# Performance work log

Measured on AMD Instinct MI355X. Metric: run time of the kernel, lower is better.

Reference implementation:

```python
import jax, jax.numpy as jnp
import numpy as np

# Production-scale dims (see shape_source)
B, D_MODEL, L = 2, 1024, 8192
NUM_GROUPS = 256          # d_model of ExplicitSingleDecayFilter
L_CACHE = 128             # explicit filter length (padded to L inside fftconv)
LOG_R_MIN, LOG_R_MAX = 0.0, 2.0  # decay_preset='strong'


def setup_inputs() -> dict:
    key = jax.random.key(0)
    k1, k2, k3, k4, k5 = jax.random.split(key, 5)
    x1 = jax.random.normal(k1, (B, D_MODEL, L), jnp.float32)
    x2 = jax.random.normal(k2, (B, D_MODEL, L), jnp.float32)
    v = jax.random.normal(k3, (B, D_MODEL, L), jnp.float32)
    # h init: randn(d_model, L_cache)/sqrt(L_cache) (small_init scale omitted for numerics)
    h = jax.random.normal(k4, (NUM_GROUPS, L_CACHE), jnp.float32) / np.sqrt(L_CACHE).astype(np.float32)
    conv_bias = jax.random.normal(k5, (D_MODEL,), jnp.float32)
    return {"x1": x1, "x2": x2, "v": v, "h": h, "conv_bias": conv_bias}


def _decay_filter(h):
    # ExplicitSingleDecayFilter: k = h * exp(-logspace(r_min, r_max)[:, None] * linspace(0, 1, L_cache)[None])
    G, Lc = h.shape
    t = jnp.linspace(0.0, 1.0, Lc, dtype=h.dtype)[None]                 # [1, Lc]
    decay_domain = jnp.logspace(LOG_R_MIN, LOG_R_MAX, G, dtype=h.dtype)[:, None]  # [G, 1]
    return h * jnp.exp(-decay_domain * t)                               # [G, Lc]


def reference(x1, x2, v, h, conv_bias):
    Bv, D, Lseq = x1.shape
    G = h.shape[0]
    gd = D // G
    fft_size = 2 * Lseq

    # grouped causal FFT convolution of the gated signal z = x2 * v
    z = (x2 * v).reshape(Bv, G, gd, Lseq)
    x1g = x1.reshape(Bv, G, gd, Lseq)

    k = _decay_filter(h)                                    # [G, L_cache]
    k = jnp.pad(k, ((0, 0), (0, Lseq - k.shape[-1])))       # pad filter to seqlen
    # torch: k_f = rfft(k, n)/n ; y = irfft(u_f*k_f, n, norm='forward')[..., :L]
    # which equals numpy-default irfft(rfft(u, n) * rfft(k, n), n)[..., :L]
    k_f = jnp.fft.rfft(k, n=fft_size)                       # [G, L+1] complex
    z_f = jnp.fft.rfft(z, n=fft_size)                       # [B, G, gd, L+1]
    y = jnp.fft.irfft(z_f * k_f[None, :, None, :], n=fft_size)[..., :Lseq]

    # D shortcut term (conv_bias), no gelu, no dropout in this operator
    Dterm = conv_bias.reshape(G, gd)
    out = y + z * Dterm[None, :, :, None]

    # post-gating by x1, back to [B, D, L] then [B, L, D]
    out = (out * x1g).reshape(Bv, D, Lseq)
    return jnp.transpose(out, (0, 2, 1))
```

## Files before the change

kernel.cpp:

```cpp
#include <hip/hip_runtime.h>

typedef float f4  __attribute__((ext_vector_type(4)));
typedef short s8v __attribute__((ext_vector_type(8)));
typedef short s4v __attribute__((ext_vector_type(4)));

#define BB    2
#define DDIM  1024
#define LSEQ  8192
#define LC    128
#define TD    16
#define TL    512
#define HALO  128
#define ZSTR  648
#define OB2   (TL/8)

__device__ __forceinline__ unsigned bf16pk(float lo, float hi) {
    unsigned a = __float_as_uint(lo), b = __float_as_uint(hi);
    a = (a + 0x7FFFu + ((a >> 16) & 1u)) >> 16;
    b = (b + 0x7FFFu + ((b >> 16) & 1u));
    return (a & 0xFFFFu) | (b & 0xFFFF0000u);
}
__device__ __forceinline__ float bf2f(short s) {
    return __uint_as_float(((unsigned)(unsigned short)s) << 16);
}

union U8 { s8v s; unsigned u[4]; };

__global__ __launch_bounds__(256, 4) void hyena_mfma_kernel(
    const float* __restrict__ x1,
    const float* __restrict__ x2,
    const float* __restrict__ v,
    const float* __restrict__ h,
    const float* __restrict__ cb,
    float* __restrict__ out)
{
    __shared__ union SM {
        short zb[TD][ZSTR];
        f4 ob[TD][OB2];
    } sm;

    const int t = threadIdx.x;

    const int flat = blockIdx.x;
    const int xcd  = flat & 7;
    const int rr_  = flat >> 3;
    const int d0   = (rr_ & 63) * TD;
    const int c_   = xcd + 8*(rr_ >> 6);
    const int l0   = (c_ & 15) * TL;
    const int b    = c_ >> 4;

    const int r = t & 15, sbase = t >> 4;
    const size_t rb = ((size_t)(b*DDIM + d0 + r)) * LSEQ;
    f4 xa0[5], xa1[5], xw0[5], xw1[5];
    #pragma unroll
    for (int it = 0; it < 5; ++it) {
        const int gl = l0 - HALO + (sbase + 16*it)*8;
        if (gl >= 0) {
            xa0[it] = *(const f4*)(x2 + rb + gl);
            xa1[it] = *(const f4*)(x2 + rb + gl + 4);
            xw0[it] = *(const f4*)(v  + rb + gl);
            xw1[it] = *(const f4*)(v  + rb + gl + 4);
        }
    }

    #pragma unroll
    for (int it = 0; it < 5; ++it) {
        const int s = sbase + 16*it;
        const int gl = l0 - HALO + s*8;
        U8 zz; zz.s = (s8v){0,0,0,0,0,0,0,0};
        if (gl >= 0) {
            const f4 z0 = xa0[it]*xw0[it], z1 = xa1[it]*xw1[it];
            zz.u[0] = bf16pk(z0[0], z0[1]);
            zz.u[1] = bf16pk(z0[2], z0[3]);
            zz.u[2] = bf16pk(z1[0], z1[1]);
            zz.u[3] = bf16pk(z1[2], z1[3]);
        }
        *(s8v*)&sm.zb[r][s*8] = zz.s;
    }

    const int wv = t >> 6, lane = t & 63;
    const int j  = lane & 15, kb = lane >> 4;
    const int qj = j & 3,  cc = j >> 2;
    const int row = wv*4 + cc;
    const size_t chb = ((size_t)(b*DDIM + d0 + row)) * LSEQ + l0;
    f4 x1r[8];
    #pragma unroll
    for (int ci = 0; ci < 8; ++ci)
        x1r[ci] = *(const f4*)(x1 + chb + 64*ci + 16*qj + 4*kb);
    const float bd = cb[d0 + row];

    const int g = (d0 >> 2) + wv;
    const float* __restrict__ hg = h + g*LC;
    const float dd = __expf((float)g * (2.0f/255.0f) * 2.302585092994046f);
    const float t0 = dd * (1.0f/127.0f);
    const int   M0base = j - 8*kb + 16;
    const float rE = __expf(t0);
    const float sU = __expf(-32.0f*t0);
    float pE[8];
    pE[0] = 1.0f;
    #pragma unroll
    for (int e = 1; e < 8; ++e) pE[e] = pE[e-1]*rE;
    float baseU = __expf(-t0*(float)M0base);

    s8v afr[5];
    #pragma unroll
    for (int u = 0; u < 5; ++u) {
        const int M0 = M0base + 32*u;
        float kv[8];
        #pragma unroll
        for (int e = 0; e < 8; ++e) {
            const int m = M0 - e;
            const int mc = m < 0 ? 0 : (m > 127 ? 127 : m);
            const float hv = hg[mc];
            const float w  = ((unsigned)m < 128u) ? baseU*pE[e] : 0.0f;
            kv[e] = hv * w;
        }
        U8 aa;
        aa.u[0] = bf16pk(kv[0], kv[1]);
        aa.u[1] = bf16pk(kv[2], kv[3]);
        aa.u[2] = bf16pk(kv[4], kv[5]);
        aa.u[3] = bf16pk(kv[6], kv[7]);
        afr[u] = aa.s;
        baseU *= sU;
    }
    __syncthreads();

    f4 ov[8];
    #pragma unroll
    for (int ci = 0; ci < 8; ++ci) {
        const int L = 64*ci + 16*qj;
        f4 acc = {0.f, 0.f, 0.f, 0.f};
        #pragma unroll
        for (int u = 0; u < 5; ++u) {
            int bi = 112 + L + 8*kb - 32*u;
            bi = bi < 0 ? 0 : bi;
            const s8v bf = *(const s8v*)&sm.zb[row][bi];
            acc = __builtin_amdgcn_mfma_f32_16x16x32_bf16(afr[u], bf, acc, 0, 0, 0);
        }
        const int lo = L + 4*kb;
        const s4v z4 = *(const s4v*)&sm.zb[row][HALO + lo];
        f4 o;
        o[0] = (acc[0] + bf2f(z4[0])*bd) * x1r[ci][0];
        o[1] = (acc[1] + bf2f(z4[1])*bd) * x1r[ci][1];
        o[2] = (acc[2] + bf2f(z4[2])*bd) * x1r[ci][2];
        o[3] = (acc[3] + bf2f(z4[3])*bd) * x1r[ci][3];
        ov[ci] = o;
    }

    const int seg = t & 3;
    #pragma unroll
    for (int hp = 0; hp < 2; ++hp) {
        __syncthreads();
        #pragma unroll
        for (int ci = 0; ci < 4; ++ci) {
            const int cidx = hp*4 + ci;
            const int J = (4*cidx + qj)*4 + kb - hp*64;
            sm.ob[row][J ^ (row & 7)] = ov[cidx];
        }
        __syncthreads();
        #pragma unroll
        for (int it = 0; it < 4; ++it) {
            const int ll = (t >> 2) + it*64;
            const int J = ll >> 2, e = ll & 3;
            f4 o;
            #pragma unroll
            for (int rr2 = 0; rr2 < 4; ++rr2) {
                const int r2 = seg*4 + rr2;
                o[rr2] = ((const float*)&sm.ob[r2][J ^ (r2 & 7)])[e];
            }
            __builtin_nontemporal_store(o,
                (f4*)(out + ((size_t)b*LSEQ + l0 + hp*256 + ll)*DDIM + d0 + seg*4));
        }
    }
}

extern "C" void kernel_launch(void* const* d_in, const int* in_sizes, int n_in,
                              void* d_out, int out_size, void* d_ws, size_t ws_size,
                              hipStream_t stream) {
    const float* x1 = (const float*)d_in[0];
    const float* x2 = (const float*)d_in[1];
    const float* v  = (const float*)d_in[2];
    const float* h  = (const float*)d_in[3];
    const float* cb = (const float*)d_in[4];
    float* outp = (float*)d_out;
    hipLaunchKernelGGL(hyena_mfma_kernel, dim3(2048), dim3(256), 0, stream,
                       x1, x2, v, h, cb, outp);
}
```

Before: 50.94 us.

## Split work into single-wave blocks of one channel group each

Each block now handles one 4-channel group with a single 64-thread wavefront instead of 16 channels across four waves. The grid grows from 2048 to 8192 blocks and shared memory per block drops, so more blocks can be resident and the block barriers only synchronise one wave. In exchange, each output store now writes 16 contiguous bytes per row instead of 64, which makes stores less coalesced, and the XOR swizzle on the staging buffer is removed.

```diff
diff --git a/kernel.cpp b/kernel.cpp
--- a/kernel.cpp
+++ b/kernel.cpp
@@ -8,11 +8,10 @@
 #define DDIM  1024
 #define LSEQ  8192
 #define LC    128
-#define TD    16
+#define TD    4
 #define TL    512
 #define HALO  128
 #define ZSTR  648
-#define OB2   (TL/8)
 
 __device__ __forceinline__ unsigned bf16pk(float lo, float hi) {
     unsigned a = __float_as_uint(lo), b = __float_as_uint(hi);
@@ -26,7 +25,7 @@
 
 union U8 { s8v s; unsigned u[4]; };
 
-__global__ __launch_bounds__(256, 4) void hyena_mfma_kernel(
+__global__ __launch_bounds__(64, 4) void hyena_mfma_kernel(
     const float* __restrict__ x1,
     const float* __restrict__ x2,
     const float* __restrict__ v,
@@ -36,7 +35,7 @@
 {
     __shared__ union SM {
         short zb[TD][ZSTR];
-        f4 ob[TD][OB2];
+        f4 ob[TD][64];
     } sm;
 
     const int t = threadIdx.x;
@@ -44,17 +43,18 @@
     const int flat = blockIdx.x;
     const int xcd  = flat & 7;
     const int rr_  = flat >> 3;
-    const int d0   = (rr_ & 63) * TD;
-    const int c_   = xcd + 8*(rr_ >> 6);
+    const int g    = rr_ & 255;
+    const int c_   = xcd + 8*(rr_ >> 8);
     const int l0   = (c_ & 15) * TL;
     const int b    = c_ >> 4;
+    const int d0   = g * 4;
 
-    const int r = t & 15, sbase = t >> 4;
+    const int r = t >> 4, sidx = t & 15;
     const size_t rb = ((size_t)(b*DDIM + d0 + r)) * LSEQ;
     f4 xa0[5], xa1[5], xw0[5], xw1[5];
     #pragma unroll
     for (int it = 0; it < 5; ++it) {
-        const int gl = l0 - HALO + (sbase + 16*it)*8;
+        const int gl = l0 - HALO + (sidx + 16*it)*8;
         if (gl >= 0) {
             xa0[it] = *(const f4*)(x2 + rb + gl);
             xa1[it] = *(const f4*)(x2 + rb + gl + 4);
@@ -65,7 +65,7 @@
 
     #pragma unroll
     for (int it = 0; it < 5; ++it) {
-        const int s = sbase + 16*it;
+        const int s = sidx + 16*it;
         const int gl = l0 - HALO + s*8;
         U8 zz; zz.s = (s8v){0,0,0,0,0,0,0,0};
         if (gl >= 0) {
@@ -78,10 +78,9 @@
         *(s8v*)&sm.zb[r][s*8] = zz.s;
     }
 
-    const int wv = t >> 6, lane = t & 63;
-    const int j  = lane & 15, kb = lane >> 4;
+    const int j  = t & 15, kb = t >> 4;
     const int qj = j & 3,  cc = j >> 2;
-    const int row = wv*4 + cc;
+    const int row = cc;
     const size_t chb = ((size_t)(b*DDIM + d0 + row)) * LSEQ + l0;
     f4 x1r[8];
     #pragma unroll
@@ -89,7 +88,6 @@
         x1r[ci] = *(const f4*)(x1 + chb + 64*ci + 16*qj + 4*kb);
     const float bd = cb[d0 + row];
 
-    const int g = (d0 >> 2) + wv;
     const float* __restrict__ hg = h + g*LC;
     const float dd = __expf((float)g * (2.0f/255.0f) * 2.302585092994046f);
     const float t0 = dd * (1.0f/127.0f);
@@ -147,7 +145,6 @@
         ov[ci] = o;
     }
 
-    const int seg = t & 3;
     #pragma unroll
     for (int hp = 0; hp < 2; ++hp) {
         __syncthreads();
@@ -155,21 +152,19 @@
         for (int ci = 0; ci < 4; ++ci) {
             const int cidx = hp*4 + ci;
             const int J = (4*cidx + qj)*4 + kb - hp*64;
-            sm.ob[row][J ^ (row & 7)] = ov[cidx];
+            sm.ob[row][J] = ov[cidx];
         }
         __syncthreads();
         #pragma unroll
         for (int it = 0; it < 4; ++it) {
-            const int ll = (t >> 2) + it*64;
+            const int ll = t + it*64;
             const int J = ll >> 2, e = ll & 3;
             f4 o;
             #pragma unroll
-            for (int rr2 = 0; rr2 < 4; ++rr2) {
-                const int r2 = seg*4 + rr2;
-                o[rr2] = ((const float*)&sm.ob[r2][J ^ (r2 & 7)])[e];
-            }
+            for (int c2 = 0; c2 < 4; ++c2)
+                o[c2] = ((const float*)&sm.ob[c2][J])[e];
             __builtin_nontemporal_store(o,
-                (f4*)(out + ((size_t)b*LSEQ + l0 + hp*256 + ll)*DDIM + d0 + seg*4));
+                (f4*)(out + ((size_t)b*LSEQ + l0 + hp*256 + ll)*DDIM + d0));
         }
     }
 }
@@ -183,6 +178,6 @@
     const float* h  = (const float*)d_in[3];
     const float* cb = (const float*)d_in[4];
     float* outp = (float*)d_out;
-    hipLaunchKernelGGL(hyena_mfma_kernel, dim3(2048), dim3(256), 0, stream,
+    hipLaunchKernelGGL(hyena_mfma_kernel, dim3(8192), dim3(64), 0, stream,
                        x1, x2, v, h, cb, outp);
 }
```

After: 169.1 us. +232.0%, slower.

## Double sequence tile per block to amortize halo and filter setup

Applied to the files above, without the earlier changes.

Each block now handles a 1024-long sequence tile instead of 512, processed as two 512 sub-tiles that share one staged z buffer and one set of filter fragments. This halves the grid, cuts the redundant 128-sample halo loads per output element, and amortizes the per-block filter construction. The z staging and output transpose buffers are no longer aliased, which raises shared memory per block, and launch bounds drop to 3 blocks per CU. That may reduce occupancy and latency hiding on a memory-bound kernel.

```diff
diff --git a/kernel.cpp b/kernel.cpp
--- a/kernel.cpp
+++ b/kernel.cpp
@@ -9,10 +9,10 @@
 #define LSEQ  8192
 #define LC    128
 #define TD    16
-#define TL    512
+#define TL    1024
 #define HALO  128
-#define ZSTR  648
-#define OB2   (TL/8)
+#define ZSTR  1160
+#define OB2   64
 
 __device__ __forceinline__ unsigned bf16pk(float lo, float hi) {
     unsigned a = __float_as_uint(lo), b = __float_as_uint(hi);
@@ -26,7 +26,7 @@
 
 union U8 { s8v s; unsigned u[4]; };
 
-__global__ __launch_bounds__(256, 4) void hyena_mfma_kernel(
+__global__ __launch_bounds__(256, 3) void hyena_mfma_kernel(
     const float* __restrict__ x1,
     const float* __restrict__ x2,
     const float* __restrict__ v,
@@ -34,10 +34,8 @@
     const float* __restrict__ cb,
     float* __restrict__ out)
 {
-    __shared__ union SM {
-        short zb[TD][ZSTR];
-        f4 ob[TD][OB2];
-    } sm;
+    __shared__ short zb[TD][ZSTR];
+    __shared__ f4    ob[TD][OB2];
 
     const int t = threadIdx.x;
 
@@ -46,50 +44,71 @@
     const int rr_  = flat >> 3;
     const int d0   = (rr_ & 63) * TD;
     const int c_   = xcd + 8*(rr_ >> 6);
-    const int l0   = (c_ & 15) * TL;
-    const int b    = c_ >> 4;
-
-    const int r = t & 15, sbase = t >> 4;
+    const int l0   = (c_ & 7) * TL;
+    const int b    = c_ >> 3;
+
+    const int r = t & 15, sidx = t >> 4;
     const size_t rb = ((size_t)(b*DDIM + d0 + r)) * LSEQ;
-    f4 xa0[5], xa1[5], xw0[5], xw1[5];
-    #pragma unroll
-    for (int it = 0; it < 5; ++it) {
-        const int gl = l0 - HALO + (sbase + 16*it)*8;
-        if (gl >= 0) {
+
+    {
+        f4 xa0[5], xa1[5], xw0[5], xw1[5];
+        #pragma unroll
+        for (int it = 0; it < 5; ++it) {
+            const int gl = l0 - HALO + (sidx + 16*it)*8;
+            if (gl >= 0) {
+                xa0[it] = *(const f4*)(x2 + rb + gl);
+                xa1[it] = *(const f4*)(x2 + rb + gl + 4);
+                xw0[it] = *(const f4*)(v  + rb + gl);
+                xw1[it] = *(const f4*)(v  + rb + gl + 4);
+            }
+        }
+        #pragma unroll
+        for (int it = 0; it < 5; ++it) {
+            const int s = sidx + 16*it;
+            const int gl = l0 - HALO + s*8;
+            U8 zz; zz.s = (s8v){0,0,0,0,0,0,0,0};
+            if (gl >= 0) {
+                const f4 z0 = xa0[it]*xw0[it], z1 = xa1[it]*xw1[it];
+                zz.u[0] = bf16pk(z0[0], z0[1]);
+                zz.u[1] = bf16pk(z0[2], z0[3]);
+                zz.u[2] = bf16pk(z1[0], z1[1]);
+                zz.u[3] = bf16pk(z1[2], z1[3]);
+            }
+            *(s8v*)&zb[r][s*8] = zz.s;
+        }
+    }
+    {
+        f4 xa0[4], xa1[4], xw0[4], xw1[4];
+        #pragma unroll
+        for (int it = 0; it < 4; ++it) {
+            const int gl = l0 - HALO + (sidx + 16*(it+5))*8;
             xa0[it] = *(const f4*)(x2 + rb + gl);
             xa1[it] = *(const f4*)(x2 + rb + gl + 4);
             xw0[it] = *(const f4*)(v  + rb + gl);
             xw1[it] = *(const f4*)(v  + rb + gl + 4);
         }
-    }
-
-    #pragma unroll
-    for (int it = 0; it < 5; ++it) {
-        const int s = sbase + 16*it;
-        const int gl = l0 - HALO + s*8;
-        U8 zz; zz.s = (s8v){0,0,0,0,0,0,0,0};
-        if (gl >= 0) {
+        #pragma unroll
+        for (int it = 0; it < 4; ++it) {
+            const int s = sidx + 16*(it+5);
             const f4 z0 = xa0[it]*xw0[it], z1 = xa1[it]*xw1[it];
+            U8 zz;
             zz.u[0] = bf16pk(z0[0], z0[1]);
             zz.u[1] = bf16pk(z0[2], z0[3]);
             zz.u[2] = bf16pk(z1[0], z1[1]);
             zz.u[3] = bf16pk(z1[2], z1[3]);
-        }
-        *(s8v*)&sm.zb[r][s*8] = zz.s;
+            *(s8v*)&zb[r][s*8] = zz.s;
+        }
     }
 
     const int wv = t >> 6, lane = t & 63;
     const int j  = lane & 15, kb = lane >> 4;
     const int qj = j & 3,  cc = j >> 2;
     const int row = wv*4 + cc;
+    const int seg = t & 3;
     const size_t chb = ((size_t)(b*DDIM + d0 + row)) * LSEQ + l0;
-    f4 x1r[8];
-    #pragma unroll
-    for (int ci = 0; ci < 8; ++ci)
-        x1r[ci] = *(const f4*)(x1 + chb + 64*ci + 16*qj + 4*kb);
     const float bd = cb[d0 + row];
-
     const int g = (d0 >> 2) + wv;
+
     const float* __restrict__ hg = h + g*LC;
     const float dd = __expf((float)g * (2.0f/255.0f) * 2.302585092994046f);
     const float t0 = dd * (1.0f/127.0f);
@@ -125,51 +144,60 @@
     }
     __syncthreads();
 
-    f4 ov[8];
     #pragma unroll
-    for (int ci = 0; ci < 8; ++ci) {
-        const int L = 64*ci + 16*qj;
-        f4 acc = {0.f, 0.f, 0.f, 0.f};
-        #pragma unroll
-        for (int u = 0; u < 5; ++u) {
-            int bi = 112 + L + 8*kb - 32*u;
-            bi = bi < 0 ? 0 : bi;
-            const s8v bf = *(const s8v*)&sm.zb[row][bi];
-            acc = __builtin_amdgcn_mfma_f32_16x16x32_bf16(afr[u], bf, acc, 0, 0, 0);
-        }
-        const int lo = L + 4*kb;
-        const s4v z4 = *(const s4v*)&sm.zb[row][HALO + lo];
-        f4 o;
-        o[0] = (acc[0] + bf2f(z4[0])*bd) * x1r[ci][0];
-        o[1] = (acc[1] + bf2f(z4[1])*bd) * x1r[ci][1];
-        o[2] = (acc[2] + bf2f(z4[2])*bd) * x1r[ci][2];
-        o[3] = (acc[3] + bf2f(z4[3])*bd) * x1r[ci][3];
-        ov[ci] = o;
-    }
-
-    const int seg = t & 3;
-    #pragma unroll
-    for (int hp = 0; hp < 2; ++hp) {
-        __syncthreads();
-        #pragma unroll
-        for (int ci = 0; ci < 4; ++ci) {
-            const int cidx = hp*4 + ci;
-            const int J = (4*cidx + qj)*4 + kb - hp*64;
-            sm.ob[row][J ^ (row & 7)] = ov[cidx];
-        }
-        __syncthreads();
-        #pragma unroll
-        for (int it = 0; it < 4; ++it) {
-            const int ll = (t >> 2) + it*64;
-            const int J = ll >> 2, e = ll & 3;
+    for (int sub = 0; sub < 2; ++sub) {
+        const int SL = sub * 512;
+
+        f4 x1r[8];
+        #pragma unroll
+        for (int ci = 0; ci < 8; ++ci)
+            x1r[ci] = *(const f4*)(x1 + chb + SL + 64*ci + 16*qj + 4*kb);
+
+        f4 ov[8];
+        #pragma unroll
+        for (int ci = 0; ci < 8; ++ci) {
+            const int L = SL + 64*ci + 16*qj;
+            f4 acc = {0.f, 0.f, 0.f, 0.f};
+            #pragma unroll
+            for (int u = 0; u < 5; ++u) {
+                int bi = 112 + L + 8*kb - 32*u;
+                bi = bi < 0 ? 0 : bi;
+                const s8v bf = *(const s8v*)&zb[row][bi];
+                acc = __builtin_amdgcn_mfma_f32_16x16x32_bf16(afr[u], bf, acc, 0, 0, 0);
+            }
+            const int lo = L + 4*kb;
+            const s4v z4 = *(const s4v*)&zb[row][HALO + lo];
             f4 o;
+            o[0] = (acc[0] + bf2f(z4[0])*bd) * x1r[ci][0];
+            o[1] = (acc[1] + bf2f(z4[1])*bd) * x1r[ci][1];
+            o[2] = (acc[2] + bf2f(z4[2])*bd) * x1r[ci][2];
+            o[3] = (acc[3] + bf2f(z4[3])*bd) * x1r[ci][3];
+            ov[ci] = o;
+        }
+
+        #pragma unroll
+        for (int hp = 0; hp < 2; ++hp) {
+            __syncthreads();
             #pragma unroll
-            for (int rr2 = 0; rr2 < 4; ++rr2) {
-                const int r2 = seg*4 + rr2;
-                o[rr2] = ((const float*)&sm.ob[r2][J ^ (r2 & 7)])[e];
-            }
-            __builtin_nontemporal_store(o,
-                (f4*)(out + ((size_t)b*LSEQ + l0 + hp*256 + ll)*DDIM + d0 + seg*4));
+            for (int ci = 0; ci < 4; ++ci) {
+                const int cidx = hp*4 + ci;
+                const int J = (4*cidx + qj)*4 + kb - hp*64;
+                ob[row][J ^ (row & 7)] = ov[cidx];
+            }
+            __syncthreads();
+            #pragma unroll
+            for (int it = 0; it < 4; ++it) {
+                const int ll = (t >> 2) + it*64;
+                const int J = ll >> 2, e = ll & 3;
+                f4 o;
+                #pragma unroll
+                for (int rr2 = 0; rr2 < 4; ++rr2) {
+                    const int r2 = seg*4 + rr2;
+                    o[rr2] = ((const float*)&ob[r2][J ^ (r2 & 7)])[e];
+                }
+                __builtin_nontemporal_store(o,
+                    (f4*)(out + ((size_t)b*LSEQ + l0 + SL + hp*256 + ll)*DDIM + d0 + seg*4));
+            }
         }
     }
 }
@@ -183,6 +211,6 @@
     const float* h  = (const float*)d_in[3];
     const float* cb = (const float*)d_in[4];
     float* outp = (float*)d_out;
-    hipLaunchKernelGGL(hyena_mfma_kernel, dim3(2048), dim3(256), 0, stream,
+    hipLaunchKernelGGL(hyena_mfma_kernel, dim3(1024), dim3(256), 0, stream,
                        x1, x2, v, h, cb, outp);
 }
```

Result: faster. 48.95 us, median of 2 (-3.9%).
